# Optimization experiments

Measured on AMD Instinct MI355X. Metric: run time of the kernel, lower is better.

The kernel has to match this reference:

```python
import jax, jax.numpy as jnp
import numpy as np

NEG_BIG = -9e15  # matches -9000000000000000.0 in the torch source
ALPHA = 0.2      # LeakyReLU negative slope


def setup_inputs() -> dict:
    key = jax.random.key(0)
    k1, k2, k3, k4 = jax.random.split(key, 4)
    N, F_in, F_out = 8192, 256, 128
    x = jax.random.normal(k1, (N, F_in), dtype=jnp.float32)
    adj = jax.random.randint(k2, (N, N), 0, 2, dtype=jnp.int32)
    W = jax.random.normal(k3, (F_in, F_out), dtype=jnp.float32) * 0.05
    a = jax.random.normal(k4, (2 * F_out, 1), dtype=jnp.float32) * 0.05
    return {"x": x, "adj": adj, "W": W, "a": a}


def reference(x, adj, W, a):
    # h = x @ W : [N, F]
    h = x @ W
    F_out = W.shape[1]
    # Algebraically identical to the concat formulation:
    # a^T [h_i || h_j] = h_i @ a1 + h_j @ a2
    a1 = a[:F_out, 0]
    a2 = a[F_out:, 0]
    src = h @ a1  # [N]
    dst = h @ a2  # [N]
    e = jax.nn.leaky_relu(src[:, None] + dst[None, :], negative_slope=ALPHA)  # [N, N]
    attention = jnp.where(adj > 0, e, NEG_BIG)
    attention = jax.nn.softmax(attention, axis=1)
    # dropout is identity in eval mode (training=False)
    h_prime = attention @ h  # [N, F]
    return h_prime
```

## Files before the change

### kernel.cpp

```cpp
#include <hip/hip_runtime.h>
#include <cstdint>

#define N 8192
#define FIN 256
#define FOUT 128
#define ALPHA 0.2f
#define JP 4
#define JSL (N / JP)
#define TJ 64
#define NTILE (JSL / TJ)
#define RB 32
#define SST 72

typedef unsigned short u16;
typedef __attribute__((ext_vector_type(8))) short short8;
typedef __attribute__((ext_vector_type(4))) float floatx4;

__device__ __forceinline__ u16 bf16_rne(float f) {
  uint32_t u = __float_as_uint(f);
  u += 0x7fff + ((u >> 16) & 1);
  return (u16)(u >> 16);
}

__device__ __forceinline__ void gl_lds16(const void* g, void* l) {
  __builtin_amdgcn_global_load_lds(
      (const __attribute__((address_space(1))) void*)g,
      (__attribute__((address_space(3))) void*)l, 16, 0, 0);
}

__global__ __launch_bounds__(256) void k_proj(const float* __restrict__ x,
                                              const float* __restrict__ W,
                                              const float* __restrict__ a,
                                              u16* __restrict__ hT3,
                                              float* __restrict__ srcv,
                                              float* __restrict__ dstv) {
  __shared__ float xs[8 * FIN];
  __shared__ float partS[4][4], partD[4][4];
  const int t = threadIdx.x;
  const int R0 = blockIdx.x * 8;

  const float4* xv = (const float4*)(x + (size_t)R0 * FIN);
  float4* xsv = (float4*)xs;
  xsv[t] = xv[t];
  xsv[t + 256] = xv[t + 256];
  __syncthreads();

  const int c  = t & 127;
  const int rg = (t >> 7) * 4;

  float acc[4] = {0.f, 0.f, 0.f, 0.f};
  float wa[4], wb[4];
  #pragma unroll
  for (int j = 0; j < 4; ++j) wa[j] = W[j * FOUT + c];
  #pragma unroll
  for (int j = 0; j < 4; ++j) wb[j] = W[(4 + j) * FOUT + c];

  for (int k4 = 0; k4 < FIN / 4; ++k4) {
    float wc[4];
    #pragma unroll
    for (int j = 0; j < 4; ++j) { wc[j] = wa[j]; wa[j] = wb[j]; }
    const int kn = (k4 + 2 < FIN / 4) ? k4 + 2 : k4;
    #pragma unroll
    for (int j = 0; j < 4; ++j) wb[j] = W[(kn * 4 + j) * FOUT + c];
    #pragma unroll
    for (int i = 0; i < 4; ++i) {
      const float4 xq = *(const float4*)&xs[(rg + i) * FIN + k4 * 4];
      acc[i] += xq.x * wc[0] + xq.y * wc[1] + xq.z * wc[2] + xq.w * wc[3];
    }
  }

  {
    const int j = R0 + rg;
    const int jb = j >> 5, q = (j >> 3) & 3, jj = j & 7;
    const int m = c & 15, nt = c >> 4;
    union { u16 u[4]; uint2 v; } pk;
    #pragma unroll
    for (int i = 0; i < 4; ++i) pk.u[i] = bf16_rne(acc[i]);
    *(uint2*)(hT3 + (size_t)(((jb * 8 + nt) * 64) + (m * 4 + q)) * 8 + jj) = pk.v;
  }

  const float a1 = a[c], a2 = a[FOUT + c];
  float s4[4], d4[4];
  #pragma unroll
  for (int i = 0; i < 4; ++i) { s4[i] = acc[i] * a1; d4[i] = acc[i] * a2; }
  #pragma unroll
  for (int off = 32; off > 0; off >>= 1) {
    #pragma unroll
    for (int i = 0; i < 4; ++i) {
      s4[i] += __shfl_down(s4[i], off);
      d4[i] += __shfl_down(d4[i], off);
    }
  }
  const int wv = t >> 6, lane = t & 63;
  if (lane == 0) {
    #pragma unroll
    for (int i = 0; i < 4; ++i) { partS[wv][i] = s4[i]; partD[wv][i] = d4[i]; }
  }
  __syncthreads();
  if (t < 16) {
    const int i = t & 3, rg2 = (t >> 2) & 1, which = t >> 3;
    if (which == 0) srcv[R0 + rg2 * 4 + i] = partS[rg2*2][i] + partS[rg2*2+1][i];
    else            dstv[R0 + rg2 * 4 + i] = partD[rg2*2][i] + partD[rg2*2+1][i];
  }
}

__global__ __launch_bounds__(256, 4) void k_gat(const int* __restrict__ adj,
                                                const u16* __restrict__ hT3,
                                                const float* __restrict__ srcv,
                                                const float* __restrict__ dstv,
                                                float* __restrict__ P,
                                                float* __restrict__ lp) {
  __shared__ u16 hS[2][8192];
  __shared__ u16 S[RB * SST];
  const int t = threadIdx.x;
  const int wv = t >> 6, lane = t & 63;
  const int q = lane >> 4, m = lane & 15;
  const int bm = blockIdx.x & 255;
  const int jp = blockIdx.x >> 8;
  const int R0 = bm * RB;
  const int j0 = jp * JSL;

  const int pr = t >> 3;
  const int pc = (t & 7) * 8;
  const float srcr = srcv[R0 + pr];
  const int*   adjp = adj + (size_t)(R0 + pr) * N + j0 + pc;
  const float* dstp = dstv + j0 + pc;

  const int rh = wv & 1, ch = wv >> 1;
  const int Lq = m * 4 + q;

  floatx4 acc[4];
  #pragma unroll
  for (int nt = 0; nt < 4; ++nt) acc[nt] = (floatx4){0.f, 0.f, 0.f, 0.f};
  float lsum = 0.f;

  const size_t jb00 = (size_t)(j0 >> 5);
  #define STAGE(I, BUF)                                                        \
  {                                                                            \
    _Pragma("unroll")                                                          \
    for (int cc = 0; cc < 4; ++cc) {                                           \
      const int kc = wv * 4 + cc;                                   \
      const int jbl = kc >> 3, nt_ = kc & 7;                                   \
      const u16* src = hT3 + ((jb00 + (size_t)(I) * 2 + jbl) * 8 + nt_) * 512  \
                       + (size_t)lane * 8;                                     \
      gl_lds16(src, &hS[BUF][kc * 512]);                                       \
    }                                                                          \
  }

  STAGE(0, 0)
  int4   aC0 = *(const int4*)(adjp),     aC1 = *(const int4*)(adjp + 4);
  float4 dC0 = *(const float4*)(dstp),   dC1 = *(const float4*)(dstp + 4);

  int buf = 0;
  for (int i = 0; i < NTILE; ++i) {
    __syncthreads();

    const int nx = (i + 1 < NTILE) ? i + 1 : i;
    if (i + 1 < NTILE) STAGE(i + 1, buf ^ 1)
    int4   aN0 = *(const int4*)(adjp + nx * TJ);
    int4   aN1 = *(const int4*)(adjp + nx * TJ + 4);
    float4 dN0 = *(const float4*)(dstp + nx * TJ);
    float4 dN1 = *(const float4*)(dstp + nx * TJ + 4);

    {
      const int   ai[8] = {aC0.x, aC0.y, aC0.z, aC0.w, aC1.x, aC1.y, aC1.z, aC1.w};
      const float df[8] = {dC0.x, dC0.y, dC0.z, dC0.w, dC1.x, dC1.y, dC1.z, dC1.w};
      union { u16 u[8]; short8 s; } pk;
      #pragma unroll
      for (int e = 0; e < 8; ++e) {
        float v = srcr + df[e];
        v = fmaxf(v, ALPHA * v);
        const float p = ai[e] > 0 ? __expf(v) : 0.f;
        lsum += p;
        pk.u[e] = bf16_rne(p);
      }
      *(short8*)&S[pr * SST + pc] = pk.s;
    }

    __syncthreads();

    {
      const short8 a0 = *(const short8*)&S[(rh * 16 + m) * SST + q * 8];
      const short8 a1 = *(const short8*)&S[(rh * 16 + m) * SST + 32 + q * 8];
      #pragma unroll
      for (int nt = 0; nt < 4; ++nt) {
        const short8 b0 = *(const short8*)&hS[buf][(0 * 8 + ch * 4 + nt) * 512 + Lq * 8];
        const short8 b1 = *(const short8*)&hS[buf][(1 * 8 + ch * 4 + nt) * 512 + Lq * 8];
        acc[nt] = __builtin_amdgcn_mfma_f32_16x16x32_bf16(a0, b0, acc[nt], 0, 0, 0);
        acc[nt] = __builtin_amdgcn_mfma_f32_16x16x32_bf16(a1, b1, acc[nt], 0, 0, 0);
      }
    }

    aC0 = aN0; aC1 = aN1; dC0 = dN0; dC1 = dN1;
    buf ^= 1;
  }
  #undef STAGE

  lsum += __shfl_down(lsum, 4);
  lsum += __shfl_down(lsum, 2);
  lsum += __shfl_down(lsum, 1);
  if ((t & 7) == 0) lp[(size_t)jp * N + R0 + pr] = lsum;

  float* Pp = P + ((size_t)jp * N + R0 + rh * 16) * FOUT + ch * 64;
  #pragma unroll
  for (int nt = 0; nt < 4; ++nt)
    #pragma unroll
    for (int ri = 0; ri < 4; ++ri)
      Pp[(size_t)(q * 4 + ri) * FOUT + nt * 16 + m] = acc[nt][ri];
}

__global__ __launch_bounds__(256) void k_norm(const float* __restrict__ P,
                                              const float* __restrict__ lp,
                                              float* __restrict__ out) {
  const int idx = blockIdx.x * 256 + threadIdx.x;
  const int rr = idx >> 5;
  const int c4 = (idx & 31) * 4;
  float l = 0.f;
  #pragma unroll
  for (int j = 0; j < JP; ++j) l += lp[j * N + rr];
  const float inv = 1.0f / l;
  float4 s = {0.f, 0.f, 0.f, 0.f};
  #pragma unroll
  for (int j = 0; j < JP; ++j) {
    const float4 p = *(const float4*)(P + ((size_t)j * N + rr) * FOUT + c4);
    s.x += p.x; s.y += p.y; s.z += p.z; s.w += p.w;
  }
  s.x *= inv; s.y *= inv; s.z *= inv; s.w *= inv;
  *(float4*)(out + (size_t)rr * FOUT + c4) = s;
}

extern "C" void kernel_launch(void* const* d_in, const int* in_sizes, int n_in,
                              void* d_out, int out_size, void* d_ws, size_t ws_size,
                              hipStream_t stream) {
  const float* x   = (const float*)d_in[0];
  const int*   adj = (const int*)d_in[1];
  const float* W   = (const float*)d_in[2];
  const float* a   = (const float*)d_in[3];
  float* out = (float*)d_out;

  char* ws = (char*)d_ws;
  u16*   hT3  = (u16*)ws;     ws += (size_t)FOUT * N * sizeof(u16);
  float* srcv = (float*)ws;   ws += (size_t)N * sizeof(float);
  float* dstv = (float*)ws;   ws += (size_t)N * sizeof(float);
  float* P    = (float*)ws;   ws += (size_t)JP * N * FOUT * sizeof(float);
  float* lp   = (float*)ws;   ws += (size_t)JP * N * sizeof(float);

  k_proj<<<N / 8, 256, 0, stream>>>(x, W, a, hT3, srcv, dstv);
  k_gat <<<256 * JP, 256, 0, stream>>>(adj, hT3, srcv, dstv, P, lp);
  k_norm<<<(N * FOUT / 4) / 256, 256, 0, stream>>>(P, lp, out);
}
```

Baseline: 435.8 us.

## Build attention MFMA operands in registers instead of staging through LDS

Each wave now computes the exp/mask attention values for its own 16 rows directly in the MFMA A-operand register layout. This removes the shared S tile, its write/read round trip and one barrier per tile. The tile loop is unrolled by two, ping-ponging the prefetched adj/dst registers. The cost is that the two column-group waves redundantly load adj and compute exp for the same rows, doubling that ALU and load work per block.

```diff
diff --git a/kernel.cpp b/kernel.cpp
--- a/kernel.cpp
+++ b/kernel.cpp
@@ -10,7 +10,6 @@
 #define TJ 64
 #define NTILE (JSL / TJ)
 #define RB 32
-#define SST 72
 
 typedef unsigned short u16;
 typedef __attribute__((ext_vector_type(8))) short short8;
@@ -111,97 +110,104 @@
                                                 float* __restrict__ P,
                                                 float* __restrict__ lp) {
   __shared__ u16 hS[2][8192];
-  __shared__ u16 S[RB * SST];
   const int t = threadIdx.x;
   const int wv = t >> 6, lane = t & 63;
   const int q = lane >> 4, m = lane & 15;
+  const int rg = wv & 1;
+  const int cg = wv >> 1;
   const int bm = blockIdx.x & 255;
   const int jp = blockIdx.x >> 8;
   const int R0 = bm * RB;
   const int j0 = jp * JSL;
-
-  const int pr = t >> 3;
-  const int pc = (t & 7) * 8;
-  const float srcr = srcv[R0 + pr];
-  const int*   adjp = adj + (size_t)(R0 + pr) * N + j0 + pc;
-  const float* dstp = dstv + j0 + pc;
-
-  const int rh = wv & 1, ch = wv >> 1;
   const int Lq = m * 4 + q;
+
+  const float srcm = srcv[R0 + rg * 16 + m];
+  const int*   adjp = adj + (size_t)(R0 + rg * 16 + m) * N + j0 + q * 8;
+  const float* dstp = dstv + j0 + q * 8;
+  const size_t jb00 = (size_t)(j0 >> 5);
 
   floatx4 acc[4];
   #pragma unroll
   for (int nt = 0; nt < 4; ++nt) acc[nt] = (floatx4){0.f, 0.f, 0.f, 0.f};
   float lsum = 0.f;
 
-  const size_t jb00 = (size_t)(j0 >> 5);
   #define STAGE(I, BUF)                                                        \
   {                                                                            \
     _Pragma("unroll")                                                          \
     for (int cc = 0; cc < 4; ++cc) {                                           \
-      const int kc = wv * 4 + cc;                                   \
+      const int kc = wv * 4 + cc;                                              \
       const int jbl = kc >> 3, nt_ = kc & 7;                                   \
-      const u16* src = hT3 + ((jb00 + (size_t)(I) * 2 + jbl) * 8 + nt_) * 512  \
-                       + (size_t)lane * 8;                                     \
-      gl_lds16(src, &hS[BUF][kc * 512]);                                       \
+      const u16* srcp = hT3 + ((jb00 + (size_t)(I) * 2 + jbl) * 8 + nt_) * 512 \
+                        + (size_t)lane * 8;                                    \
+      gl_lds16(srcp, &hS[BUF][kc * 512]);                                      \
     }                                                                          \
   }
 
+  #define TILE_BODY(I, BUFR, BUFW,                                             \
+                    CA0, CA1, CA2, CA3, CD0, CD1, CD2, CD3,                    \
+                    NA0, NA1, NA2, NA3, ND0, ND1, ND2, ND3)                    \
+  {                                                                            \
+    __syncthreads();        \
+    const int nx = ((I) + 1 < NTILE) ? (I) + 1 : (I);                          \
+    NA0 = *(const int4*)(adjp + nx * TJ);                                      \
+    NA1 = *(const int4*)(adjp + nx * TJ + 4);                                  \
+    NA2 = *(const int4*)(adjp + nx * TJ + 32);                                 \
+    NA3 = *(const int4*)(adjp + nx * TJ + 36);                                 \
+    ND0 = *(const float4*)(dstp + nx * TJ);                                    \
+    ND1 = *(const float4*)(dstp + nx * TJ + 4);                                \
+    ND2 = *(const float4*)(dstp + nx * TJ + 32);                               \
+    ND3 = *(const float4*)(dstp + nx * TJ + 36);                               \
+    STAGE(nx, BUFW)                                                            \
+    _Pragma("unroll")                                                          \
+    for (int ks = 0; ks < 2; ++ks) {                                           \
+      const int4   A0 = ks ? CA2 : CA0, A1 = ks ? CA3 : CA1;                   \
+      const float4 D0 = ks ? CD2 : CD0, D1 = ks ? CD3 : CD1;                   \
+      const int   ai[8] = {A0.x, A0.y, A0.z, A0.w, A1.x, A1.y, A1.z, A1.w};    \
+      const float df[8] = {D0.x, D0.y, D0.z, D0.w, D1.x, D1.y, D1.z, D1.w};    \
+      union { u16 u[8]; short8 s; } pk;                                        \
+      _Pragma("unroll")                                                        \
+      for (int e = 0; e < 8; ++e) {                                            \
+        float v = srcm + df[e];                                                \
+        v = fmaxf(v, ALPHA * v);                                               \
+        const float p = ai[e] > 0 ? __expf(v) : 0.f;                           \
+        lsum += p;                                                             \
+        pk.u[e] = bf16_rne(p);                                                 \
+      }                                                                        \
+      _Pragma("unroll")                                                        \
+      for (int nt = 0; nt < 4; ++nt) {                                         \
+        const short8 bf =                                                      \
+            *(const short8*)&hS[BUFR][(ks * 8 + cg * 4 + nt) * 512 + Lq * 8];  \
+        acc[nt] =                                                              \
+            __builtin_amdgcn_mfma_f32_16x16x32_bf16(pk.s, bf, acc[nt], 0, 0, 0); \
+      }                                                                        \
+    }                                                                          \
+  }
+
+  int4   aA0 = *(const int4*)(adjp),      aA1 = *(const int4*)(adjp + 4);
+  int4   aA2 = *(const int4*)(adjp + 32), aA3 = *(const int4*)(adjp + 36);
+  float4 dA0 = *(const float4*)(dstp),      dA1 = *(const float4*)(dstp + 4);
+  float4 dA2 = *(const float4*)(dstp + 32), dA3 = *(const float4*)(dstp + 36);
   STAGE(0, 0)
-  int4   aC0 = *(const int4*)(adjp),     aC1 = *(const int4*)(adjp + 4);
-  float4 dC0 = *(const float4*)(dstp),   dC1 = *(const float4*)(dstp + 4);
-
-  int buf = 0;
-  for (int i = 0; i < NTILE; ++i) {
-    __syncthreads();
-
-    const int nx = (i + 1 < NTILE) ? i + 1 : i;
-    if (i + 1 < NTILE) STAGE(i + 1, buf ^ 1)
-    int4   aN0 = *(const int4*)(adjp + nx * TJ);
-    int4   aN1 = *(const int4*)(adjp + nx * TJ + 4);
-    float4 dN0 = *(const float4*)(dstp + nx * TJ);
-    float4 dN1 = *(const float4*)(dstp + nx * TJ + 4);
-
-    {
-      const int   ai[8] = {aC0.x, aC0.y, aC0.z, aC0.w, aC1.x, aC1.y, aC1.z, aC1.w};
-      const float df[8] = {dC0.x, dC0.y, dC0.z, dC0.w, dC1.x, dC1.y, dC1.z, dC1.w};
-      union { u16 u[8]; short8 s; } pk;
-      #pragma unroll
-      for (int e = 0; e < 8; ++e) {
-        float v = srcr + df[e];
-        v = fmaxf(v, ALPHA * v);
-        const float p = ai[e] > 0 ? __expf(v) : 0.f;
-        lsum += p;
-        pk.u[e] = bf16_rne(p);
-      }
-      *(short8*)&S[pr * SST + pc] = pk.s;
-    }
-
-    __syncthreads();
-
-    {
-      const short8 a0 = *(const short8*)&S[(rh * 16 + m) * SST + q * 8];
-      const short8 a1 = *(const short8*)&S[(rh * 16 + m) * SST + 32 + q * 8];
-      #pragma unroll
-      for (int nt = 0; nt < 4; ++nt) {
-        const short8 b0 = *(const short8*)&hS[buf][(0 * 8 + ch * 4 + nt) * 512 + Lq * 8];
-        const short8 b1 = *(const short8*)&hS[buf][(1 * 8 + ch * 4 + nt) * 512 + Lq * 8];
-        acc[nt] = __builtin_amdgcn_mfma_f32_16x16x32_bf16(a0, b0, acc[nt], 0, 0, 0);
-        acc[nt] = __builtin_amdgcn_mfma_f32_16x16x32_bf16(a1, b1, acc[nt], 0, 0, 0);
-      }
-    }
-
-    aC0 = aN0; aC1 = aN1; dC0 = dN0; dC1 = dN1;
-    buf ^= 1;
-  }
+  int4   aB0, aB1, aB2, aB3;
+  float4 dB0, dB1, dB2, dB3;
+
+  for (int i = 0; i < NTILE; i += 2) {
+    TILE_BODY(i,     (i >> 1) & 0 ? 1 : 0, 1,
+              aA0, aA1, aA2, aA3, dA0, dA1, dA2, dA3,
+              aB0, aB1, aB2, aB3, dB0, dB1, dB2, dB3)
+    TILE_BODY(i + 1, 1, 0,
+              aB0, aB1, aB2, aB3, dB0, dB1, dB2, dB3,
+              aA0, aA1, aA2, aA3, dA0, dA1, dA2, dA3)
+  }
+  #undef TILE_BODY
   #undef STAGE
 
-  lsum += __shfl_down(lsum, 4);
-  lsum += __shfl_down(lsum, 2);
-  lsum += __shfl_down(lsum, 1);
-  if ((t & 7) == 0) lp[(size_t)jp * N + R0 + pr] = lsum;
-
-  float* Pp = P + ((size_t)jp * N + R0 + rh * 16) * FOUT + ch * 64;
+  lsum += __shfl_xor(lsum, 16);
+  lsum += __shfl_xor(lsum, 32);
+  if (cg == 0 && lane < 16)
+    lp[(size_t)jp * N + R0 + rg * 16 + lane] = lsum;
+
+  float* Pp = P + ((size_t)jp * N + R0 + rg * 16) * FOUT + cg * 64;
   #pragma unroll
   for (int nt = 0; nt < 4; ++nt)
     #pragma unroll
```

After: 456.7 us. 1.05x slower.

## Split fused attention kernel into probability-generation and bf16 MFMA matmul kernels

Applied to the files above, without the earlier changes.

The fused kernel that computed masked exp probabilities and multiplied them by h in one pass is replaced by two kernels. The first writes the full bf16 probability matrix (N x N) in MFMA fragment layout plus row sums. The second streams those fragments and h tiles into LDS with global_load_lds and runs a double-buffered MFMA loop, with a 2-way split over K instead of 4. This takes the exp/compare work and the adj loads off the MFMA critical path, but adds a 128 MB intermediate write and read-back to global memory.

```diff
diff --git a/kernel.cpp b/kernel.cpp
--- a/kernel.cpp
+++ b/kernel.cpp
@@ -5,12 +5,6 @@
 #define FIN 256
 #define FOUT 128
 #define ALPHA 0.2f
-#define JP 4
-#define JSL (N / JP)
-#define TJ 64
-#define NTILE (JSL / TJ)
-#define RB 32
-#define SST 72
 
 typedef unsigned short u16;
 typedef __attribute__((ext_vector_type(8))) short short8;
@@ -104,128 +98,137 @@
   }
 }
 
-__global__ __launch_bounds__(256, 4) void k_gat(const int* __restrict__ adj,
-                                                const u16* __restrict__ hT3,
-                                                const float* __restrict__ srcv,
-                                                const float* __restrict__ dstv,
-                                                float* __restrict__ P,
-                                                float* __restrict__ lp) {
-  __shared__ u16 hS[2][8192];
-  __shared__ u16 S[RB * SST];
-  const int t = threadIdx.x;
-  const int wv = t >> 6, lane = t & 63;
-  const int q = lane >> 4, m = lane & 15;
-  const int bm = blockIdx.x & 255;
-  const int jp = blockIdx.x >> 8;
-  const int R0 = bm * RB;
-  const int j0 = jp * JSL;
-
-  const int pr = t >> 3;
-  const int pc = (t & 7) * 8;
-  const float srcr = srcv[R0 + pr];
-  const int*   adjp = adj + (size_t)(R0 + pr) * N + j0 + pc;
-  const float* dstp = dstv + j0 + pc;
-
-  const int rh = wv & 1, ch = wv >> 1;
-  const int Lq = m * 4 + q;
-
-  floatx4 acc[4];
-  #pragma unroll
-  for (int nt = 0; nt < 4; ++nt) acc[nt] = (floatx4){0.f, 0.f, 0.f, 0.f};
+__global__ __launch_bounds__(256) void k_pgen(const int* __restrict__ adj,
+                                              const float* __restrict__ srcv,
+                                              const float* __restrict__ dstv,
+                                              u16* __restrict__ Pt,
+                                              float* __restrict__ lp) {
+  const int t  = threadIdx.x;
+  const int rb = blockIdx.x >> 1;
+  const int jh = blockIdx.x & 1;
+  const int R0 = rb * 16;
+  const int j0 = jh * 4096;
+  const int m  = t >> 4;
+  const int sx = t & 15;
+
+  const float srcr = srcv[R0 + m];
+  const int*   ap = adj + (size_t)(R0 + m) * N + j0 + sx * 4;
+  const float* dp = dstv + j0 + sx * 4;
+  u16* pp = Pt + ((size_t)(rb * 256 + jh * 128 + (sx >> 3)) * 512)
+               + m * 32 + ((sx & 7) * 4);
+
   float lsum = 0.f;
-
-  const size_t jb00 = (size_t)(j0 >> 5);
+  #pragma unroll 4
+  for (int kp = 0; kp < 64; ++kp) {
+    const int4   A = *(const int4*)(ap + kp * 64);
+    const float4 D = *(const float4*)(dp + kp * 64);
+    const int   ai[4] = {A.x, A.y, A.z, A.w};
+    const float df[4] = {D.x, D.y, D.z, D.w};
+    union { u16 u[4]; uint2 v; } pk;
+    #pragma unroll
+    for (int e = 0; e < 4; ++e) {
+      float v = srcr + df[e];
+      v = fmaxf(v, ALPHA * v);
+      const float p = ai[e] > 0 ? __expf(v) : 0.f;
+      lsum += p;
+      pk.u[e] = bf16_rne(p);
+    }
+    *(uint2*)(pp + (size_t)kp * 1024) = pk.v;
+  }
+
+  lsum += __shfl_xor(lsum, 1);
+  lsum += __shfl_xor(lsum, 2);
+  lsum += __shfl_xor(lsum, 4);
+  lsum += __shfl_xor(lsum, 8);
+  if (sx == 0) lp[(size_t)jh * N + R0 + m] = lsum;
+}
+
+__global__ __launch_bounds__(256, 4) void k_av(const u16* __restrict__ Pt,
+                                               const u16* __restrict__ hT3,
+                                               float* __restrict__ P2) {
+  __shared__ u16 aS[2][4 * 512];
+  __shared__ u16 bS[2][8 * 512];
+  const int t = threadIdx.x, wv = t >> 6, lane = t & 63;
+  const int q = lane >> 4, m = lane & 15, Lq = m * 4 + q;
+  const int rb32 = blockIdx.x >> 2;
+  const int ch   = (blockIdx.x >> 1) & 1;
+  const int ksp  = blockIdx.x & 1;
+  const int R0 = rb32 * 32;
+  const int kb0 = ksp * 128;
+  const int rh = wv & 1, ntp = wv >> 1;
+
+  floatx4 acc[2];
+  acc[0] = (floatx4){0.f, 0.f, 0.f, 0.f};
+  acc[1] = (floatx4){0.f, 0.f, 0.f, 0.f};
+
   #define STAGE(I, BUF)                                                        \
   {                                                                            \
     _Pragma("unroll")                                                          \
-    for (int cc = 0; cc < 4; ++cc) {                                           \
-      const int kc = wv * 4 + cc;                                   \
-      const int jbl = kc >> 3, nt_ = kc & 7;                                   \
-      const u16* src = hT3 + ((jb00 + (size_t)(I) * 2 + jbl) * 8 + nt_) * 512  \
+    for (int cc = 0; cc < 3; ++cc) {                                           \
+      const int d = wv * 3 + cc;                                               \
+      if (d < 4) {                                                             \
+        const int rr = d >> 1, kk = d & 1;                                     \
+        const u16* s = Pt + ((size_t)((rb32 * 2 + rr) * 256 + kb0 + (I) * 2 + kk)) * 512 \
                        + (size_t)lane * 8;                                     \
-      gl_lds16(src, &hS[BUF][kc * 512]);                                       \
+        gl_lds16(s, &aS[BUF][d * 512]);                                        \
+      } else {                                                                 \
+        const int e = d - 4, jbx = e >> 2, nn = e & 3;                         \
+        const u16* s = hT3 + ((size_t)(kb0 + (I) * 2 + jbx) * 8 + ch * 4 + nn) * 512 \
+                       + (size_t)lane * 8;                                     \
+        gl_lds16(s, &bS[BUF][e * 512]);                                        \
+      }                                                                        \
     }                                                                          \
   }
 
+  #define MFMA_TILE(BUF)                                                       \
+  {                                                                            \
+    _Pragma("unroll")                                                          \
+    for (int kk = 0; kk < 2; ++kk) {                                           \
+      const short8 af = *(const short8*)&aS[BUF][(rh * 2 + kk) * 512 + Lq * 8];\
+      _Pragma("unroll")                                                        \
+      for (int nn = 0; nn < 2; ++nn) {                                         \
+        const short8 bf =                                                      \
+            *(const short8*)&bS[BUF][(kk * 4 + ntp * 2 + nn) * 512 + Lq * 8];  \
+        acc[nn] = __builtin_amdgcn_mfma_f32_16x16x32_bf16(af, bf, acc[nn], 0, 0, 0); \
+      }                                                                        \
+    }                                                                          \
+  }
+
   STAGE(0, 0)
-  int4   aC0 = *(const int4*)(adjp),     aC1 = *(const int4*)(adjp + 4);
-  float4 dC0 = *(const float4*)(dstp),   dC1 = *(const float4*)(dstp + 4);
-
-  int buf = 0;
-  for (int i = 0; i < NTILE; ++i) {
+  for (int i = 0; i < 64; i += 2) {
     __syncthreads();
-
-    const int nx = (i + 1 < NTILE) ? i + 1 : i;
-    if (i + 1 < NTILE) STAGE(i + 1, buf ^ 1)
-    int4   aN0 = *(const int4*)(adjp + nx * TJ);
-    int4   aN1 = *(const int4*)(adjp + nx * TJ + 4);
-    float4 dN0 = *(const float4*)(dstp + nx * TJ);
-    float4 dN1 = *(const float4*)(dstp + nx * TJ + 4);
-
-    {
-      const int   ai[8] = {aC0.x, aC0.y, aC0.z, aC0.w, aC1.x, aC1.y, aC1.z, aC1.w};
-      const float df[8] = {dC0.x, dC0.y, dC0.z, dC0.w, dC1.x, dC1.y, dC1.z, dC1.w};
-      union { u16 u[8]; short8 s; } pk;
-      #pragma unroll
-      for (int e = 0; e < 8; ++e) {
-        float v = srcr + df[e];
-        v = fmaxf(v, ALPHA * v);
-        const float p = ai[e] > 0 ? __expf(v) : 0.f;
-        lsum += p;
-        pk.u[e] = bf16_rne(p);
-      }
-      *(short8*)&S[pr * SST + pc] = pk.s;
-    }
-
+    { const int nx = (i + 1 < 64) ? i + 1 : i; STAGE(nx, 1) }
+    MFMA_TILE(0)
     __syncthreads();
-
-    {
-      const short8 a0 = *(const short8*)&S[(rh * 16 + m) * SST + q * 8];
-      const short8 a1 = *(const short8*)&S[(rh * 16 + m) * SST + 32 + q * 8];
-      #pragma unroll
-      for (int nt = 0; nt < 4; ++nt) {
-        const short8 b0 = *(const short8*)&hS[buf][(0 * 8 + ch * 4 + nt) * 512 + Lq * 8];
-        const short8 b1 = *(const short8*)&hS[buf][(1 * 8 + ch * 4 + nt) * 512 + Lq * 8];
-        acc[nt] = __builtin_amdgcn_mfma_f32_16x16x32_bf16(a0, b0, acc[nt], 0, 0, 0);
-        acc[nt] = __builtin_amdgcn_mfma_f32_16x16x32_bf16(a1, b1, acc[nt], 0, 0, 0);
-      }
-    }
-
-    aC0 = aN0; aC1 = aN1; dC0 = dN0; dC1 = dN1;
-    buf ^= 1;
+    { const int nx = (i + 2 < 64) ? i + 2 : i + 1; STAGE(nx, 0) }
+    MFMA_TILE(1)
   }
   #undef STAGE
-
-  lsum += __shfl_down(lsum, 4);
-  lsum += __shfl_down(lsum, 2);
-  lsum += __shfl_down(lsum, 1);
-  if ((t & 7) == 0) lp[(size_t)jp * N + R0 + pr] = lsum;
-
-  float* Pp = P + ((size_t)jp * N + R0 + rh * 16) * FOUT + ch * 64;
-  #pragma unroll
-  for (int nt = 0; nt < 4; ++nt)
+  #undef MFMA_TILE
+  __syncthreads();
+
+  float* Pp = P2 + ((size_t)ksp * N + R0 + rh * 16) * FOUT + ch * 64 + ntp * 32 + m;
+  #pragma unroll
+  for (int nn = 0; nn < 2; ++nn)
     #pragma unroll
     for (int ri = 0; ri < 4; ++ri)
-      Pp[(size_t)(q * 4 + ri) * FOUT + nt * 16 + m] = acc[nt][ri];
-}
-
-__global__ __launch_bounds__(256) void k_norm(const float* __restrict__ P,
+      Pp[(size_t)(q * 4 + ri) * FOUT + nn * 16] = acc[nn][ri];
+}
+
+__global__ __launch_bounds__(256) void k_norm(const float* __restrict__ P2,
                                               const float* __restrict__ lp,
                                               float* __restrict__ out) {
   const int idx = blockIdx.x * 256 + threadIdx.x;
   const int rr = idx >> 5;
   const int c4 = (idx & 31) * 4;
-  float l = 0.f;
-  #pragma unroll
-  for (int j = 0; j < JP; ++j) l += lp[j * N + rr];
-  const float inv = 1.0f / l;
-  float4 s = {0.f, 0.f, 0.f, 0.f};
-  #pragma unroll
-  for (int j = 0; j < JP; ++j) {
-    const float4 p = *(const float4*)(P + ((size_t)j * N + rr) * FOUT + c4);
-    s.x += p.x; s.y += p.y; s.z += p.z; s.w += p.w;
-  }
-  s.x *= inv; s.y *= inv; s.z *= inv; s.w *= inv;
+  const float inv = 1.0f / (lp[rr] + lp[N + rr]);
+  const float4 p0 = *(const float4*)(P2 + (size_t)rr * FOUT + c4);
+  const float4 p1 = *(const float4*)(P2 + ((size_t)N + rr) * FOUT + c4);
+  float4 s;
+  s.x = (p0.x + p1.x) * inv;
+  s.y = (p0.y + p1.y) * inv;
+  s.z = (p0.z + p1.z) * inv;
+  s.w = (p0.w + p1.w) * inv;
   *(float4*)(out + (size_t)rr * FOUT + c4) = s;
 }
 
@@ -242,10 +245,12 @@
   u16*   hT3  = (u16*)ws;     ws += (size_t)FOUT * N * sizeof(u16);
   float* srcv = (float*)ws;   ws += (size_t)N * sizeof(float);
   float* dstv = (float*)ws;   ws += (size_t)N * sizeof(float);
-  float* P    = (float*)ws;   ws += (size_t)JP * N * FOUT * sizeof(float);
-  float* lp   = (float*)ws;   ws += (size_t)JP * N * sizeof(float);
+  u16*   Pt   = (u16*)ws;     ws += (size_t)N * N * sizeof(u16);
+  float* lp   = (float*)ws;   ws += (size_t)2 * N * sizeof(float);
+  float* P2   = (float*)ws;   ws += (size_t)2 * N * FOUT * sizeof(float);
 
   k_proj<<<N / 8, 256, 0, stream>>>(x, W, a, hT3, srcv, dstv);
-  k_gat <<<256 * JP, 256, 0, stream>>>(adj, hT3, srcv, dstv, P, lp);
-  k_norm<<<(N * FOUT / 4) / 256, 256, 0, stream>>>(P, lp, out);
-}
+  k_pgen<<<1024, 256, 0, stream>>>(adj, srcv, dstv, Pt, lp);
+  k_av  <<<1024, 256, 0, stream>>>(Pt, hT3, P2);
+  k_norm<<<(N * FOUT / 4) / 256, 256, 0, stream>>>(P2, lp, out);
+}
```

Result: slower. 472.8 us (+8.5%).
